# Kernel optimization log

Hardware: AMD Instinct MI355X
Metric: run time of the kernel (lower is better)

The kernel has to match this reference:

```python
import jax, jax.numpy as jnp
import numpy as np

B, C, H, W = 4, 64, 128, 128
O, K = 64, 3
STRIDE, PAD = 1, 1
K2 = K * K


def conv2d(x, w, b):
    out = jax.lax.conv_general_dilated(
        x, w, (STRIDE, STRIDE), [(PAD, PAD), (PAD, PAD)],
        dimension_numbers=('NCHW', 'OIHW', 'NCHW'))
    return out + b[None, :, None, None]


def setup_inputs() -> dict:
    key = jax.random.key(0)
    ks = jax.random.split(key, 6)
    return {
        'x': jax.random.normal(ks[0], (B, C, H, W), jnp.float32),
        'offset_w': jax.random.normal(ks[1], (2 * K2, C, K, K), jnp.float32) * 0.01,
        'offset_b': jax.random.normal(ks[2], (2 * K2,), jnp.float32) * 0.01,
        'mask_w': jax.random.normal(ks[3], (K2, C, K, K), jnp.float32) * 0.01,
        'mask_b': jnp.zeros((K2,), jnp.float32),
        'deform_w': jax.random.normal(ks[4], (O, C, K, K), jnp.float32) * (1.0 / np.sqrt(C * K2)),
        'deform_b': jax.random.normal(ks[5], (O,), jnp.float32) * 0.01,
    }


def _deform_conv(x, offset, mask, w, b):
    Bn, Cn, Hin, Win = x.shape
    Ho, Wo = offset.shape[2], offset.shape[3]
    off = offset.reshape(Bn, K2, 2, Ho, Wo)
    ky = jnp.repeat(jnp.arange(K), K)   # kernel row offset per location k
    kx = jnp.tile(jnp.arange(K), K)     # kernel col offset per location k
    yo = jnp.arange(Ho) * STRIDE - PAD
    xo = jnp.arange(Wo) * STRIDE - PAD
    # sampling positions [B,K2,Ho,Wo]
    py = off[:, :, 0] + ky[None, :, None, None] + yo[None, None, :, None]
    px = off[:, :, 1] + kx[None, :, None, None] + xo[None, None, None, :]
    y0 = jnp.floor(py)
    x0 = jnp.floor(px)
    wy1 = py - y0  # fractional weights
    wx1 = px - x0
    y0i = y0.astype(jnp.int32)
    x0i = x0.astype(jnp.int32)
    x_flat = x.reshape(Bn, Cn, Hin * Win)

    def corner(yi, xi, wgt):
        valid = (yi >= 0) & (yi < Hin) & (xi >= 0) & (xi < Win)
        yc = jnp.clip(yi, 0, Hin - 1)
        xc = jnp.clip(xi, 0, Win - 1)
        idx = (yc * Win + xc).reshape(Bn, -1)
        g = jnp.take_along_axis(x_flat, idx[:, None, :], axis=2)
        g = g.reshape(Bn, Cn, K2, Ho, Wo)
        return g * (wgt * valid)[:, None]

    val = (corner(y0i, x0i, (1 - wy1) * (1 - wx1))
           + corner(y0i, x0i + 1, (1 - wy1) * wx1)
           + corner(y0i + 1, x0i, wy1 * (1 - wx1))
           + corner(y0i + 1, x0i + 1, wy1 * wx1))
    val = val * mask[:, None]  # modulate, broadcast over channels
    out = jnp.einsum('bckhw,ock->bohw', val, w.reshape(w.shape[0], Cn, K2))
    return out + b[None, :, None, None]


def reference(x, offset_w, offset_b, mask_w, mask_b, deform_w, deform_b):
    offset = conv2d(x, offset_w, offset_b)
    mask = jax.nn.sigmoid(conv2d(x, mask_w, mask_b))
    return _deform_conv(x, offset, mask, deform_w, deform_b)
```

## Files before the change

kernel.cpp:

```cpp
#include <hip/hip_runtime.h>
#include <hip/hip_bf16.h>
#include <math.h>

#define BB 4
#define CC 64
#define HH 128
#define WW 128
#define HW 16384
#define CHW (CC*HW)

typedef __bf16 bf16;
typedef __attribute__((ext_vector_type(8))) __bf16 bf16x8;
typedef __attribute__((ext_vector_type(4))) __bf16 bf16x4;
typedef __attribute__((ext_vector_type(4))) float f32x4;
typedef __attribute__((ext_vector_type(4))) unsigned short u16x4;

#define MFMA(a, b, c) __builtin_amdgcn_mfma_f32_16x16x32_bf16((a), (b), (c), 0, 0, 0)

__global__ __launch_bounds__(256) void k_pre(const float* __restrict__ x,
        bf16* __restrict__ xt,
        const float* __restrict__ dw, const float* __restrict__ ow,
        const float* __restrict__ mw,
        bf16* __restrict__ wfd_hi,
        bf16* __restrict__ wfo_hi, bf16* __restrict__ wfo_lo) {
    __shared__ float tile[64][65];
    if (blockIdx.x < 1024) {
        int b  = blockIdx.x >> 8;
        int s0 = (blockIdx.x & 255) * 64;
        int t  = threadIdx.x;
        const float* xb = x + (size_t)b * CHW;
        int sl = (t & 15) * 4;
        int c0 = t >> 4;
        #pragma unroll
        for (int r = 0; r < 4; ++r) {
            int c = c0 + r * 16;
            float4 v = *(const float4*)&xb[(size_t)c * HW + s0 + sl];
            tile[c][sl]     = v.x;
            tile[c][sl + 1] = v.y;
            tile[c][sl + 2] = v.z;
            tile[c][sl + 3] = v.w;
        }
        __syncthreads();
        int lane = t & 63, w = t >> 6;
        int si = w * 16 + (lane >> 2);
        int cg = (lane & 3) * 16;
        bf16x8 h0, h1;
        #pragma unroll
        for (int j = 0; j < 8; ++j) {
            h0[j] = (bf16)tile[cg + j][si];
            h1[j] = (bf16)tile[cg + 8 + j][si];
        }
        bf16* dst = xt + (size_t)b * CHW + (size_t)(s0 + si) * 64 + cg;
        *(bf16x8*)dst       = h0;
        *(bf16x8*)(dst + 8) = h1;
    } else {
        int idx = (blockIdx.x - 1024) * 256 + threadIdx.x;
        if (idx < 36864) {
            int j    = idx & 7;
            int lane = (idx >> 3) & 63;
            int ks   = (idx >> 9) % 18;
            int nt   = idx / (512 * 18);
            int n    = nt * 16 + (lane & 15);
            int kglob = ks * 32 + (lane >> 4) * 8 + j;
            int kk = kglob >> 6, c = kglob & 63;
            wfd_hi[idx] = (bf16)dw[(n * 64 + c) * 9 + kk];
        } else {
            int idx2 = idx - 36864;
            int j    = idx2 & 7;
            int lane = (idx2 >> 3) & 63;
            int ks   = (idx2 >> 9) % 18;
            int nt   = idx2 / (512 * 18);
            int ch   = nt * 16 + (lane & 15);
            int kglob = ks * 32 + (lane >> 4) * 8 + j;
            int kk = kglob >> 6, c = kglob & 63;
            float w = 0.0f;
            if (ch < 18)      w = ow[(ch * 64 + c) * 9 + kk];
            else if (ch < 27) w = mw[((ch - 18) * 64 + c) * 9 + kk];
            bf16 h = (bf16)w;
            wfo_hi[idx2] = h;
            wfo_lo[idx2] = (bf16)(w - (float)h);
        }
    }
}

__global__ __launch_bounds__(256) void k_offmask(const bf16* __restrict__ xt,
        const bf16* __restrict__ wfo_hi, const bf16* __restrict__ wfo_lo,
        const float* __restrict__ ob, const float* __restrict__ mb,
        bf16* __restrict__ sampw_g, unsigned short* __restrict__ sampo_g) {
    __shared__ float om_s[27 * 64];

    int pos0 = blockIdx.x * 64;
    int wo0 = pos0 & 127;
    int ho  = (pos0 >> 7) & 127;
    int b   = pos0 >> 14;
    int t = threadIdx.x, wave = t >> 6, lane = t & 63;
    int m = lane & 15, g = lane >> 4;
    const bf16* xtb = xt + (size_t)b * CHW;

    {
        int st = wave;
        f32x4 acc0 = {0.f, 0.f, 0.f, 0.f};
        f32x4 acc1 = {0.f, 0.f, 0.f, 0.f};
        const bf16x8* bh0 = (const bf16x8*)wfo_hi + lane;
        const bf16x8* bl0 = (const bf16x8*)wfo_lo + lane;
        const bf16x8* bh1 = (const bf16x8*)wfo_hi + 18 * 64 + lane;
        const bf16x8* bl1 = (const bf16x8*)wfo_lo + 18 * 64 + lane;
        #pragma unroll
        for (int kk = 0; kk < 9; ++kk) {
            int y  = ho + kk / 3 - 1;
            int xx = wo0 + st * 16 + m + (kk % 3) - 1;
            bf16x8 ae = {};
            bf16x8 ao = {};
            if ((unsigned)y < 128u && (unsigned)xx < 128u) {
                const bf16* bp = xtb + ((size_t)(y * 128 + xx) << 6);
                ae = *(const bf16x8*)(bp + g * 8);
                ao = *(const bf16x8*)(bp + 32 + g * 8);
            }
            int ks0 = 2 * kk, ks1 = 2 * kk + 1;
            acc0 = MFMA(ae, bh0[ks0 * 64], acc0);
            acc0 = MFMA(ae, bl0[ks0 * 64], acc0);
            acc0 = MFMA(ao, bh0[ks1 * 64], acc0);
            acc0 = MFMA(ao, bl0[ks1 * 64], acc0);
            acc1 = MFMA(ae, bh1[ks0 * 64], acc1);
            acc1 = MFMA(ae, bl1[ks0 * 64], acc1);
            acc1 = MFMA(ao, bh1[ks1 * 64], acc1);
            acc1 = MFMA(ao, bl1[ks1 * 64], acc1);
        }
        int p64 = st * 16 + g * 4;
        float bias0 = ob[m];
        #pragma unroll
        for (int r = 0; r < 4; ++r)
            om_s[m * 64 + p64 + r] = acc0[r] + bias0;
        int ch1 = 16 + m;
        if (ch1 < 27) {
            float bias1 = (ch1 < 18) ? ob[ch1] : mb[ch1 - 18];
            #pragma unroll
            for (int r = 0; r < 4; ++r) {
                float v = acc1[r] + bias1;
                if (ch1 >= 18) v = 1.0f / (1.0f + __expf(-v));
                om_s[ch1 * 64 + p64 + r] = v;
            }
        }
    }
    __syncthreads();

    for (int tl = t; tl < 576; tl += 256) {
        int p64 = tl / 9, k = tl - p64 * 9;
        float dy = om_s[(2 * k) * 64 + p64];
        float dx = om_s[(2 * k + 1) * 64 + p64];
        float mk = om_s[(18 + k) * 64 + p64];
        float py = (float)(ho - 1 + k / 3) + dy;
        float px = (float)(wo0 + p64 - 1 + (k % 3)) + dx;
        float y0f = floorf(py), x0f = floorf(px);
        float fy = py - y0f, fx = px - x0f;
        int y0 = (int)y0f, x0 = (int)x0f;
        int y1 = y0 + 1,  x1 = x0 + 1;
        bool vy0 = (unsigned)y0 < 128u, vy1 = (unsigned)y1 < 128u;
        bool vx0 = (unsigned)x0 < 128u, vx1 = (unsigned)x1 < 128u;
        int y0c = min(max(y0, 0), 127), y1c = min(max(y1, 0), 127);
        int x0c = min(max(x0, 0), 127), x1c = min(max(x1, 0), 127);
        bf16x4 wv;
        wv.x = (bf16)((vy0 && vx0) ? mk * (1.f - fy) * (1.f - fx) : 0.f);
        wv.y = (bf16)((vy0 && vx1) ? mk * (1.f - fy) * fx         : 0.f);
        wv.z = (bf16)((vy1 && vx0) ? mk * fy * (1.f - fx)         : 0.f);
        wv.w = (bf16)((vy1 && vx1) ? mk * fy * fx                 : 0.f);
        u16x4 ov;
        ov.x = (unsigned short)(y0c * 128 + x0c);
        ov.y = (unsigned short)(y0c * 128 + x1c);
        ov.z = (unsigned short)(y1c * 128 + x0c);
        ov.w = (unsigned short)(y1c * 128 + x1c);
        int gtask = pos0 * 9 + tl;
        *(bf16x4*)&sampw_g[gtask * 4] = wv;
        *(u16x4*)&sampo_g[gtask * 4] = ov;
    }
}

__global__ __launch_bounds__(256, 4) void k_deform(const bf16* __restrict__ xt,
        const bf16* __restrict__ wfd_hi,
        const bf16* __restrict__ sampw_g, const unsigned short* __restrict__ sampo_g,
        const float* __restrict__ db, float* __restrict__ out) {
    __shared__ __align__(16) char stage[4 * 2 * 16 * 144];

    int t = threadIdx.x, wave = t >> 6, lane = t & 63;
    int m = lane & 15, g = lane >> 4;
    int p16  = blockIdx.x * 4 + wave;
    int pos0 = p16 * 16;
    int wo0 = pos0 & 127;
    int ho  = (pos0 >> 7) & 127;
    int b   = pos0 >> 14;
    const bf16* xtb = xt + (size_t)b * CHW;
    char* mybuf = stage + wave * (2 * 16 * 144);

    f32x4 acc[4];
    #pragma unroll
    for (int nt = 0; nt < 4; ++nt) acc[nt] = (f32x4){0.f, 0.f, 0.f, 0.f};
    const bf16x8* bhd = (const bf16x8*)wfd_hi + lane;
    int cq8 = m * 8;

    for (int kk = 0; kk < 9; ++kk) {
        char* buf = mybuf + (kk & 1) * (16 * 144);
        #pragma unroll
        for (int it = 0; it < 4; ++it) {
            int s = it * 4 + g;
            int gtask = (pos0 + s) * 9 + kk;
            bf16x4 wb = *(const bf16x4*)&sampw_g[gtask * 4];
            u16x4  o4 = *(const u16x4*)&sampo_g[gtask * 4];
            bf16x4 c0 = *(const bf16x4*)(xtb + ((int)o4.x << 6) + m * 4);
            bf16x4 c1 = *(const bf16x4*)(xtb + ((int)o4.y << 6) + m * 4);
            bf16x4 c2 = *(const bf16x4*)(xtb + ((int)o4.z << 6) + m * 4);
            bf16x4 c3 = *(const bf16x4*)(xtb + ((int)o4.w << 6) + m * 4);
            float w00 = (float)wb.x, w01 = (float)wb.y;
            float w10 = (float)wb.z, w11 = (float)wb.w;
            float r0 = w00 * (float)c0.x + w01 * (float)c1.x + w10 * (float)c2.x + w11 * (float)c3.x;
            float r1 = w00 * (float)c0.y + w01 * (float)c1.y + w10 * (float)c2.y + w11 * (float)c3.y;
            float r2 = w00 * (float)c0.z + w01 * (float)c1.z + w10 * (float)c2.z + w11 * (float)c3.z;
            float r3 = w00 * (float)c0.w + w01 * (float)c1.w + w10 * (float)c2.w + w11 * (float)c3.w;
            bf16x4 hv = {(bf16)r0, (bf16)r1, (bf16)r2, (bf16)r3};
            *(bf16x4*)(buf + s * 144 + cq8) = hv;
        }
        bf16x8 a0 = *(const bf16x8*)(buf + m * 144 + g * 16);
        bf16x8 a1 = *(const bf16x8*)(buf + m * 144 + 64 + g * 16);
        int ks0 = 2 * kk, ks1 = ks0 + 1;
        #pragma unroll
        for (int nt = 0; nt < 4; ++nt) {
            acc[nt] = MFMA(a0, bhd[(nt * 18 + ks0) * 64], acc[nt]);
            acc[nt] = MFMA(a1, bhd[(nt * 18 + ks1) * 64], acc[nt]);
        }
    }

    #pragma unroll
    for (int nt = 0; nt < 4; ++nt) {
        int o = nt * 16 + m;
        float bias = db[o];
        float4 vv = {acc[nt][0] + bias, acc[nt][1] + bias,
                     acc[nt][2] + bias, acc[nt][3] + bias};
        *(float4*)&out[((size_t)(b * 64 + o)) * HW + ho * 128 + wo0 + g * 4] = vv;
    }
}

extern "C" void kernel_launch(void* const* d_in, const int* in_sizes, int n_in,
                              void* d_out, int out_size, void* d_ws, size_t ws_size,
                              hipStream_t stream) {
    const float* x   = (const float*)d_in[0];
    const float* ow  = (const float*)d_in[1];
    const float* ob  = (const float*)d_in[2];
    const float* mw  = (const float*)d_in[3];
    const float* mb  = (const float*)d_in[4];
    const float* dw  = (const float*)d_in[5];
    const float* db  = (const float*)d_in[6];
    float* out = (float*)d_out;

    bf16* xt      = (bf16*)d_ws;
    bf16* wfd_hi  = xt + (size_t)BB * HW * CC;
    bf16* wfo_hi  = wfd_hi + 36864;
    bf16* wfo_lo  = wfo_hi + 18432;
    bf16* sampw_g = wfo_lo + 18432;
    unsigned short* sampo_g = (unsigned short*)(sampw_g + (size_t)589824 * 4);

    k_pre<<<1024 + 216, 256, 0, stream>>>(x, xt, dw, ow, mw, wfd_hi, wfo_hi, wfo_lo);
    k_offmask<<<(BB * HW) / 64, 256, 0, stream>>>(xt, wfo_hi, wfo_lo, ob, mb, sampw_g, sampo_g);
    k_deform<<<(BB * HW) / 64, 256, 0, stream>>>(xt, wfd_hi, sampw_g, sampo_g, db, out);
}
```

Baseline: 140.4 us.

## Pack sample records and software-pipeline deform gathers across kernel taps

Merges the per-tap bilinear weights and corner offsets into one 16-byte record, so each sample is fetched with a single vector load instead of two. The deform kernel becomes one wave per block, and its tap loop is fully unrolled. It prefetches the next tap's corner gathers and the records two taps ahead into registers while the current tap is blended and fed to MFMA. This is meant to hide gather latency, at the cost of much higher register pressure and smaller blocks with launch bounds (64,3).

```diff
diff --git a/kernel.cpp b/kernel.cpp
--- a/kernel.cpp
+++ b/kernel.cpp
@@ -16,6 +16,11 @@
 typedef __attribute__((ext_vector_type(4))) unsigned short u16x4;
 
 #define MFMA(a, b, c) __builtin_amdgcn_mfma_f32_16x16x32_bf16((a), (b), (c), 0, 0, 0)
+
+union PRec {
+    float4 f;
+    struct { bf16x4 wb; unsigned short o[4]; } s;
+};
 
 __global__ __launch_bounds__(256) void k_pre(const float* __restrict__ x,
         bf16* __restrict__ xt,
@@ -86,7 +91,7 @@
 __global__ __launch_bounds__(256) void k_offmask(const bf16* __restrict__ xt,
         const bf16* __restrict__ wfo_hi, const bf16* __restrict__ wfo_lo,
         const float* __restrict__ ob, const float* __restrict__ mb,
-        bf16* __restrict__ sampw_g, unsigned short* __restrict__ sampo_g) {
+        float4* __restrict__ samp_g) {
     __shared__ float om_s[27 * 64];
 
     int pos0 = blockIdx.x * 64;
@@ -159,64 +164,81 @@
         bool vx0 = (unsigned)x0 < 128u, vx1 = (unsigned)x1 < 128u;
         int y0c = min(max(y0, 0), 127), y1c = min(max(y1, 0), 127);
         int x0c = min(max(x0, 0), 127), x1c = min(max(x1, 0), 127);
-        bf16x4 wv;
-        wv.x = (bf16)((vy0 && vx0) ? mk * (1.f - fy) * (1.f - fx) : 0.f);
-        wv.y = (bf16)((vy0 && vx1) ? mk * (1.f - fy) * fx         : 0.f);
-        wv.z = (bf16)((vy1 && vx0) ? mk * fy * (1.f - fx)         : 0.f);
-        wv.w = (bf16)((vy1 && vx1) ? mk * fy * fx                 : 0.f);
-        u16x4 ov;
-        ov.x = (unsigned short)(y0c * 128 + x0c);
-        ov.y = (unsigned short)(y0c * 128 + x1c);
-        ov.z = (unsigned short)(y1c * 128 + x0c);
-        ov.w = (unsigned short)(y1c * 128 + x1c);
-        int gtask = pos0 * 9 + tl;
-        *(bf16x4*)&sampw_g[gtask * 4] = wv;
-        *(u16x4*)&sampo_g[gtask * 4] = ov;
-    }
-}
-
-__global__ __launch_bounds__(256, 4) void k_deform(const bf16* __restrict__ xt,
+        PRec r;
+        r.s.wb.x = (bf16)((vy0 && vx0) ? mk * (1.f - fy) * (1.f - fx) : 0.f);
+        r.s.wb.y = (bf16)((vy0 && vx1) ? mk * (1.f - fy) * fx         : 0.f);
+        r.s.wb.z = (bf16)((vy1 && vx0) ? mk * fy * (1.f - fx)         : 0.f);
+        r.s.wb.w = (bf16)((vy1 && vx1) ? mk * fy * fx                 : 0.f);
+        r.s.o[0] = (unsigned short)(y0c * 128 + x0c);
+        r.s.o[1] = (unsigned short)(y0c * 128 + x1c);
+        r.s.o[2] = (unsigned short)(y1c * 128 + x0c);
+        r.s.o[3] = (unsigned short)(y1c * 128 + x1c);
+        samp_g[pos0 * 9 + tl] = r.f;
+    }
+}
+
+__global__ __launch_bounds__(64, 3) void k_deform(const bf16* __restrict__ xt,
         const bf16* __restrict__ wfd_hi,
-        const bf16* __restrict__ sampw_g, const unsigned short* __restrict__ sampo_g,
+        const float4* __restrict__ samp_g,
         const float* __restrict__ db, float* __restrict__ out) {
-    __shared__ __align__(16) char stage[4 * 2 * 16 * 144];
-
-    int t = threadIdx.x, wave = t >> 6, lane = t & 63;
+    __shared__ __align__(16) char stage[2 * 16 * 144];
+
+    int lane = threadIdx.x;
     int m = lane & 15, g = lane >> 4;
-    int p16  = blockIdx.x * 4 + wave;
-    int pos0 = p16 * 16;
+    int pos0 = blockIdx.x * 16;
     int wo0 = pos0 & 127;
     int ho  = (pos0 >> 7) & 127;
     int b   = pos0 >> 14;
     const bf16* xtb = xt + (size_t)b * CHW;
-    char* mybuf = stage + wave * (2 * 16 * 144);
+    const float4* sp = samp_g + (size_t)pos0 * 9;
+    int cq = m * 4;
 
     f32x4 acc[4];
     #pragma unroll
     for (int nt = 0; nt < 4; ++nt) acc[nt] = (f32x4){0.f, 0.f, 0.f, 0.f};
     const bf16x8* bhd = (const bf16x8*)wfd_hi + lane;
-    int cq8 = m * 8;
-
-    for (int kk = 0; kk < 9; ++kk) {
-        char* buf = mybuf + (kk & 1) * (16 * 144);
+
+    PRec pp0[4], pp1[4];
+    bf16x4 cr0[4][4], cr1[4][4];
+
+    #pragma unroll
+    for (int it = 0; it < 4; ++it) pp0[it].f = sp[(it * 4 + g) * 9 + 0];
+    #pragma unroll
+    for (int it = 0; it < 4; ++it) {
+        #pragma unroll
+        for (int c = 0; c < 4; ++c)
+            cr0[it][c] = *(const bf16x4*)(xtb + ((int)pp0[it].s.o[c] << 6) + cq);
+    }
+    #pragma unroll
+    for (int it = 0; it < 4; ++it) pp1[it].f = sp[(it * 4 + g) * 9 + 1];
+
+    auto stageFn = [&](int kk, PRec (&PPc)[4], bf16x4 (&CRc)[4][4],
+                       PRec (&PPn)[4], bf16x4 (&CRn)[4][4]) {
+        char* buf = stage + (kk & 1) * 2304;
+        if (kk + 1 < 9) {
+            #pragma unroll
+            for (int it = 0; it < 4; ++it) {
+                #pragma unroll
+                for (int c = 0; c < 4; ++c)
+                    CRn[it][c] = *(const bf16x4*)(xtb + ((int)PPn[it].s.o[c] << 6) + cq);
+            }
+        }
         #pragma unroll
         for (int it = 0; it < 4; ++it) {
-            int s = it * 4 + g;
-            int gtask = (pos0 + s) * 9 + kk;
-            bf16x4 wb = *(const bf16x4*)&sampw_g[gtask * 4];
-            u16x4  o4 = *(const u16x4*)&sampo_g[gtask * 4];
-            bf16x4 c0 = *(const bf16x4*)(xtb + ((int)o4.x << 6) + m * 4);
-            bf16x4 c1 = *(const bf16x4*)(xtb + ((int)o4.y << 6) + m * 4);
-            bf16x4 c2 = *(const bf16x4*)(xtb + ((int)o4.z << 6) + m * 4);
-            bf16x4 c3 = *(const bf16x4*)(xtb + ((int)o4.w << 6) + m * 4);
+            bf16x4 wb = PPc[it].s.wb;
             float w00 = (float)wb.x, w01 = (float)wb.y;
             float w10 = (float)wb.z, w11 = (float)wb.w;
+            bf16x4 c0 = CRc[it][0], c1 = CRc[it][1], c2 = CRc[it][2], c3 = CRc[it][3];
             float r0 = w00 * (float)c0.x + w01 * (float)c1.x + w10 * (float)c2.x + w11 * (float)c3.x;
             float r1 = w00 * (float)c0.y + w01 * (float)c1.y + w10 * (float)c2.y + w11 * (float)c3.y;
             float r2 = w00 * (float)c0.z + w01 * (float)c1.z + w10 * (float)c2.z + w11 * (float)c3.z;
             float r3 = w00 * (float)c0.w + w01 * (float)c1.w + w10 * (float)c2.w + w11 * (float)c3.w;
             bf16x4 hv = {(bf16)r0, (bf16)r1, (bf16)r2, (bf16)r3};
-            *(bf16x4*)(buf + s * 144 + cq8) = hv;
+            *(bf16x4*)(buf + (it * 4 + g) * 144 + m * 8) = hv;
+        }
+        if (kk + 2 < 9) {
+            #pragma unroll
+            for (int it = 0; it < 4; ++it) PPc[it].f = sp[(it * 4 + g) * 9 + kk + 2];
         }
         bf16x8 a0 = *(const bf16x8*)(buf + m * 144 + g * 16);
         bf16x8 a1 = *(const bf16x8*)(buf + m * 144 + 64 + g * 16);
@@ -226,6 +248,12 @@
             acc[nt] = MFMA(a0, bhd[(nt * 18 + ks0) * 64], acc[nt]);
             acc[nt] = MFMA(a1, bhd[(nt * 18 + ks1) * 64], acc[nt]);
         }
+    };
+
+    #pragma unroll
+    for (int kk = 0; kk < 9; ++kk) {
+        if (kk & 1) stageFn(kk, pp1, cr1, pp0, cr0);
+        else        stageFn(kk, pp0, cr0, pp1, cr1);
     }
 
     #pragma unroll
@@ -254,10 +282,9 @@
     bf16* wfd_hi  = xt + (size_t)BB * HW * CC;
     bf16* wfo_hi  = wfd_hi + 36864;
     bf16* wfo_lo  = wfo_hi + 18432;
-    bf16* sampw_g = wfo_lo + 18432;
-    unsigned short* sampo_g = (unsigned short*)(sampw_g + (size_t)589824 * 4);
+    float4* samp_g = (float4*)(wfo_lo + 18432 + 8);
 
     k_pre<<<1024 + 216, 256, 0, stream>>>(x, xt, dw, ow, mw, wfd_hi, wfo_hi, wfo_lo);
-    k_offmask<<<(BB * HW) / 64, 256, 0, stream>>>(xt, wfo_hi, wfo_lo, ob, mb, sampw_g, sampo_g);
-    k_deform<<<(BB * HW) / 64, 256, 0, stream>>>(xt, wfd_hi, sampw_g, sampo_g, db, out);
-}
+    k_offmask<<<(BB * HW) / 64, 256, 0, stream>>>(xt, wfo_hi, wfo_lo, ob, mb, samp_g);
+    k_deform<<<(BB * HW) / 16, 64, 0, stream>>>(xt, wfd_hi, samp_g, db, out);
+}
```

New measurement: 135.7 us. 3.4% less time.
